# Performance work log

Measured on AMD Instinct MI355X. Metric: run time of the kernel, lower is better.

Reference implementation:

```python
import jax, jax.numpy as jnp
import numpy as np

EPS = 1e-5


def _bn(h, gamma, beta):
    # BatchNorm1d in training mode: batch statistics over node dim
    mu = h.mean(axis=0)
    var = h.var(axis=0)
    return gamma * (h - mu) * jax.lax.rsqrt(var + EPS) + beta


def _rgcn_layer(x, src, dst, etype, W, Wloop, b, n_dst):
    # Relation-specific gather-transform-scatter (DGL RelGraphConv, sum agg,
    # self-loop + bias, no regularizer).
    x_src = x[src]                                   # [E, in] gather
    num_rels = W.shape[0]
    m = jnp.zeros((x_src.shape[0], W.shape[2]), x.dtype)
    for r in range(num_rels):                        # small fixed relation count
        m = m + jnp.where((etype == r)[:, None], x_src @ W[r], 0.0)
    agg = jax.ops.segment_sum(m, dst, num_segments=n_dst)  # scatter-add to dst
    # DGL block convention: dst nodes are the prefix of src nodes
    return agg + x[:n_dst] @ Wloop + b


def setup_inputs() -> dict:
    key = jax.random.key(0)
    ks = jax.random.split(key, 16)
    N_SRC, N_DST0, N_DST1 = 200000, 50000, 10000
    E0, E1, R, H, C = 800000, 160000, 5, 256, 153
    s = 1.0 / np.sqrt(H)
    inp = {
        "x": jax.random.normal(ks[0], (N_SRC, H), jnp.float32),
        "src0": jax.random.randint(ks[1], (E0,), 0, N_SRC, jnp.int32),
        "dst0": jax.random.randint(ks[2], (E0,), 0, N_DST0, jnp.int32),
        "etype0": jax.random.randint(ks[3], (E0,), 0, R, jnp.int32),
        "src1": jax.random.randint(ks[4], (E1,), 0, N_DST0, jnp.int32),
        "dst1": jax.random.randint(ks[5], (E1,), 0, N_DST1, jnp.int32),
        "etype1": jax.random.randint(ks[6], (E1,), 0, R, jnp.int32),
        "n_dst0": N_DST0,
        "n_dst1": N_DST1,
        "W0": jax.random.normal(ks[7], (R, H, H), jnp.float32) * s,
        "Wl0": jax.random.normal(ks[8], (H, H), jnp.float32) * s,
        "b0": jnp.zeros((H,), jnp.float32),
        "g0": jnp.ones((H,), jnp.float32),
        "be0": jnp.zeros((H,), jnp.float32),
        "W1": jax.random.normal(ks[9], (R, H, H), jnp.float32) * s,
        "Wl1": jax.random.normal(ks[10], (H, H), jnp.float32) * s,
        "b1": jnp.zeros((H,), jnp.float32),
        "g1": jnp.ones((H,), jnp.float32),
        "be1": jnp.zeros((H,), jnp.float32),
        "Wm1": jax.random.normal(ks[11], (H, H), jnp.float32) * s,
        "bm1": jnp.zeros((H,), jnp.float32),
        "gm": jnp.ones((H,), jnp.float32),
        "bem": jnp.zeros((H,), jnp.float32),
        "Wm2": jax.random.normal(ks[12], (H, C), jnp.float32) * s,
        "bm2": jnp.zeros((C,), jnp.float32),
    }
    return inp


def reference(x, src0, dst0, etype0, src1, dst1, etype1, n_dst0, n_dst1,
              W0, Wl0, b0, g0, be0, W1, Wl1, b1, g1, be1,
              Wm1, bm1, gm, bem, Wm2, bm2):
    # layer 0
    h = _rgcn_layer(x, src0, dst0, etype0, W0, Wl0, b0, n_dst0)
    h = jax.nn.elu(_bn(h, g0, be0))
    # layer 1
    h = _rgcn_layer(h, src1, dst1, etype1, W1, Wl1, b1, n_dst1)
    h = jax.nn.elu(_bn(h, g1, be1))
    # MLP head (dropout is identity in eval)
    h = jax.nn.relu(_bn(h @ Wm1 + bm1, gm, bem))
    return h @ Wm2 + bm2
```

## Files before the change

### kernel.cpp

```cpp
#include <hip/hip_runtime.h>
#include <hip/hip_bf16.h>


#define HD   256
#define EPS  1e-5f
#define NREL 5
#define ND0  50000
#define ND1  10000
#define BK   64

typedef unsigned short ushort_t;
using f32x4  = __attribute__((ext_vector_type(4))) float;
using short8 = __attribute__((ext_vector_type(8))) short;

__device__ __forceinline__ ushort_t f2b(float f) {
    union { float f; unsigned u; } x; x.f = f;
    unsigned r = x.u + 0x7FFF + ((x.u >> 16) & 1);
    return (ushort_t)(r >> 16);
}
__device__ __forceinline__ float b2f(ushort_t h) {
    union { unsigned u; float f; } x; x.u = ((unsigned)h) << 16;
    return x.f;
}

#define GLOAD_LDS16(gp, lp)                                                     \
    __builtin_amdgcn_global_load_lds(                                           \
        (const __attribute__((address_space(1))) unsigned int*)(gp),            \
        (__attribute__((address_space(3))) unsigned int*)(lp), 16, 0, 0)

struct WconvArgs {
    const float* src[14];
    ushort_t*    dst[14];
    int          N[14];
};
__global__ void wconv_all_kernel(WconvArgs a) {
    int mat = blockIdx.x >> 8;
    int id = (blockIdx.x & 255) * 256 + threadIdx.x;
    int n = id >> 8, k = id & 255;
    int N = a.N[mat];
    float v = (n < N) ? a.src[mat][(size_t)k * N + n] : 0.f;
    a.dst[mat][id] = f2b(v);
}

__global__ void xconv_kernel(const float* __restrict__ x, ushort_t* __restrict__ xb,
                             int n4) {
    int id = blockIdx.x * 256 + threadIdx.x;
    if (id >= n4) return;
    float4 v = ((const float4*)x)[id];
    ushort4 o; o.x = f2b(v.x); o.y = f2b(v.y); o.z = f2b(v.z); o.w = f2b(v.w);
    ((ushort4*)xb)[id] = o;
}

__global__ void count2_kernel(const int* __restrict__ d0, const int* __restrict__ e0, int E0,
                              const int* __restrict__ d1, const int* __restrict__ e1, int E1,
                              int* __restrict__ cnt, int* __restrict__ pos) {
    int e = blockIdx.x * 256 + threadIdx.x;
    if (e < E0) {
        pos[e] = atomicAdd(&cnt[e0[e] * ND0 + d0[e]], 1);
    } else if (e < E0 + E1) {
        int i = e - E0;
        pos[e] = atomicAdd(&cnt[NREL * ND0 + e1[i] * ND1 + d1[i]], 1);
    }
}

__global__ void scan_block_kernel(const int* __restrict__ in, int* __restrict__ out,
                                  int* __restrict__ bsum, int nb) {
    __shared__ int ts[256];
    int tid = threadIdx.x;
    int base = blockIdx.x * 1024 + tid * 4;
    int v0 = (base + 0 < nb) ? in[base + 0] : 0;
    int v1 = (base + 1 < nb) ? in[base + 1] : 0;
    int v2 = (base + 2 < nb) ? in[base + 2] : 0;
    int v3 = (base + 3 < nb) ? in[base + 3] : 0;
    int tsum = v0 + v1 + v2 + v3;
    ts[tid] = tsum;
    __syncthreads();
    for (int d = 1; d < 256; d <<= 1) {
        int t = (tid >= d) ? ts[tid - d] : 0;
        __syncthreads();
        ts[tid] += t;
        __syncthreads();
    }
    int excl = ts[tid] - tsum;
    if (base + 0 < nb) out[base + 0] = excl;
    if (base + 1 < nb) out[base + 1] = excl + v0;
    if (base + 2 < nb) out[base + 2] = excl + v0 + v1;
    if (base + 3 < nb) out[base + 3] = excl + v0 + v1 + v2;
    if (tid == 255 && bsum) bsum[blockIdx.x] = ts[255];
}

__global__ void scan_add_kernel(int* __restrict__ out, const int* __restrict__ bsum, int nb) {
    int i = blockIdx.x * 256 + threadIdx.x;
    if (i < nb) out[i] += bsum[i >> 10];
}

__global__ void fill2_kernel(const int* __restrict__ s0, const int* __restrict__ d0,
                             const int* __restrict__ e0, int E0,
                             const int* __restrict__ s1, const int* __restrict__ d1,
                             const int* __restrict__ e1, int E1,
                             const int* __restrict__ pos, const int* __restrict__ off,
                             int* __restrict__ ssrc) {
    int e = blockIdx.x * 256 + threadIdx.x;
    if (e < E0) {
        ssrc[off[e0[e] * ND0 + d0[e]] + pos[e]] = s0[e];
    } else if (e < E0 + E1) {
        int i = e - E0;
        ssrc[off[NREL * ND0 + e1[i] * ND1 + d1[i]] + pos[e]] = s1[i];
    }
}

__global__ void gather_kernel(const ushort_t* __restrict__ feat, const int* __restrict__ ssrc,
                              const int* __restrict__ cnt, const int* __restrict__ off,
                              int nbuckets, ushort_t* __restrict__ out,
                              const float* __restrict__ sc, const float* __restrict__ sh) {
    int wave = (blockIdx.x * 256 + threadIdx.x) >> 6;
    int lane = threadIdx.x & 63;
    if (wave >= nbuckets) return;
    int deg = cnt[wave], s = off[wave];
    int half = lane >> 5;
    int cl = lane & 31;
    float a[8] = {0.f, 0.f, 0.f, 0.f, 0.f, 0.f, 0.f, 0.f};
    if (sc) {
        float4 s0v = ((const float4*)sc)[cl * 2], s1v = ((const float4*)sc)[cl * 2 + 1];
        float4 h0v = ((const float4*)sh)[cl * 2], h1v = ((const float4*)sh)[cl * 2 + 1];
        float scv[8] = {s0v.x, s0v.y, s0v.z, s0v.w, s1v.x, s1v.y, s1v.z, s1v.w};
        float shv[8] = {h0v.x, h0v.y, h0v.z, h0v.w, h1v.x, h1v.y, h1v.z, h1v.w};
        int j = half;
        for (; j + 2 < deg; j += 4) {
            int r0 = ssrc[s + j], r1 = ssrc[s + j + 2];
            uint4 v0 = *(const uint4*)(feat + (size_t)r0 * HD + cl * 8);
            uint4 v1 = *(const uint4*)(feat + (size_t)r1 * HD + cl * 8);
            const ushort_t* u0 = (const ushort_t*)&v0;
            const ushort_t* u1 = (const ushort_t*)&v1;
#pragma unroll
            for (int i = 0; i < 8; i++) {
                float f0 = fmaf(b2f(u0[i]), scv[i], shv[i]);
                float f1 = fmaf(b2f(u1[i]), scv[i], shv[i]);
                a[i] += (f0 > 0.f ? f0 : expm1f(f0)) + (f1 > 0.f ? f1 : expm1f(f1));
            }
        }
        if (j < deg) {
            int r = ssrc[s + j];
            uint4 v = *(const uint4*)(feat + (size_t)r * HD + cl * 8);
            const ushort_t* u = (const ushort_t*)&v;
#pragma unroll
            for (int i = 0; i < 8; i++) {
                float f = fmaf(b2f(u[i]), scv[i], shv[i]);
                a[i] += f > 0.f ? f : expm1f(f);
            }
        }
    } else {
        int j = half;
        for (; j + 2 < deg; j += 4) {
            int r0 = ssrc[s + j], r1 = ssrc[s + j + 2];
            uint4 v0 = *(const uint4*)(feat + (size_t)r0 * HD + cl * 8);
            uint4 v1 = *(const uint4*)(feat + (size_t)r1 * HD + cl * 8);
            const ushort_t* u0 = (const ushort_t*)&v0;
            const ushort_t* u1 = (const ushort_t*)&v1;
#pragma unroll
            for (int i = 0; i < 8; i++) a[i] += b2f(u0[i]) + b2f(u1[i]);
        }
        if (j < deg) {
            int r = ssrc[s + j];
            uint4 v = *(const uint4*)(feat + (size_t)r * HD + cl * 8);
            const ushort_t* u = (const ushort_t*)&v;
#pragma unroll
            for (int i = 0; i < 8; i++) a[i] += b2f(u[i]);
        }
    }
#pragma unroll
    for (int i = 0; i < 8; i++) a[i] += __shfl_xor(a[i], 32);
    if (half == 0) {
        ushort_t o[8];
#pragma unroll
        for (int i = 0; i < 8; i++) o[i] = f2b(a[i]);
        *(uint4*)(out + (size_t)wave * HD + cl * 8) = *(const uint4*)o;
    }
}

__global__ void bnprep_kernel(const float* __restrict__ sums, const float* __restrict__ g,
                              const float* __restrict__ be, float invM,
                              float* __restrict__ sc, float* __restrict__ sh) {
    int c = threadIdx.x;
    float mu = sums[c] * invM;
    float var = sums[HD + c] * invM - mu * mu;
    float s = g[c] * rsqrtf(var + EPS);
    sc[c] = s; sh[c] = be[c] - mu * s;
}

struct Seg {
    const ushort_t* A;
    const ushort_t* B;
    const float* sc;
    const float* sh;
    int act;
};
struct GemmArgs {
    Seg seg[6];
    int nseg;
    const float* bias;
    float* stats;
    ushort_t* Cb;
    float* Cf;
    int M, N;
};

template <int BM>
__launch_bounds__(256, 4)
__global__ void gemm_mfma_kernel(GemmArgs g) {
    constexpr int F   = BM / 32;
    constexpr int NFT = BM / 16;
    constexpr int IT  = NFT * 2 / 4;
    __shared__ __align__(1024) ushort_t As[NFT * 2 * 512];
    __shared__ __align__(1024) ushort_t Bs[NFT * 2 * 512];
    int tid = threadIdx.x;
    int wave = tid >> 6, lane = tid & 63;
    int rq = lane >> 4, ci = lane & 15;
    int wm = (wave >> 1) * (BM / 2), wn = (wave & 1) * (BM / 2);
    int bm = blockIdx.y * BM, bn = blockIdx.x * BM;
    f32x4 acc[F][F] = {};
    int K = g.nseg * HD;

    for (int kk = 0; kk < K; kk += BK) {
        int si = kk >> 8;
        int kl = kk & 255;
        const ushort_t* Ap = g.seg[si].A;
        const ushort_t* Bp = g.seg[si].B;
        const float* sc = g.seg[si].sc;
        if (!sc) {
#pragma unroll
            for (int it = 0; it < IT; it++) {
                int f = it * 4 + wave;
                int mt = f >> 1, kt = f & 1;
                const ushort_t* ga = Ap + (size_t)(bm + mt * 16 + ci) * HD
                                        + kl + kt * 32 + rq * 8;
                GLOAD_LDS16(ga, &As[f * 512 + lane * 8]);
            }
        } else {
            const float* sh = g.seg[si].sh;
            int act = g.seg[si].act;
#pragma unroll
            for (int it = 0; it < IT; it++) {
                int f = it * 4 + wave;
                int mt = f >> 1, kt = f & 1;
                int kb = kl + kt * 32 + rq * 8;
                uint4 v = *(const uint4*)(Ap + (size_t)(bm + mt * 16 + ci) * HD + kb);
                ushort_t* u = (ushort_t*)&v;
#pragma unroll
                for (int j = 0; j < 8; j++) {
                    float fv = fmaf(b2f(u[j]), sc[kb + j], sh[kb + j]);
                    fv = (act == 2) ? fmaxf(fv, 0.f) : (fv > 0.f ? fv : expm1f(fv));
                    u[j] = f2b(fv);
                }
                *(uint4*)&As[f * 512 + lane * 8] = v;
            }
        }
#pragma unroll
        for (int it = 0; it < IT; it++) {
            int f = it * 4 + wave;
            int nt = f >> 1, kt = f & 1;
            const ushort_t* gb = Bp + (size_t)(bn + nt * 16 + ci) * HD
                                    + kl + kt * 32 + rq * 8;
            GLOAD_LDS16(gb, &Bs[f * 512 + lane * 8]);
        }
        __syncthreads();
#pragma unroll
        for (int ks = 0; ks < 2; ks++) {
            short8 a[F], b[F];
#pragma unroll
            for (int mi = 0; mi < F; mi++)
                a[mi] = *(const short8*)&As[((wm / 16 + mi) * 2 + ks) * 512 + lane * 8];
#pragma unroll
            for (int ni = 0; ni < F; ni++)
                b[ni] = *(const short8*)&Bs[((wn / 16 + ni) * 2 + ks) * 512 + lane * 8];
#pragma unroll
            for (int mi = 0; mi < F; mi++)
#pragma unroll
                for (int ni = 0; ni < F; ni++)
                    acc[mi][ni] = __builtin_amdgcn_mfma_f32_16x16x32_bf16(
                        a[mi], b[ni], acc[mi][ni], 0, 0, 0);
        }
        __syncthreads();
    }

#pragma unroll
    for (int ni = 0; ni < F; ni++) {
        int col = bn + wn + ni * 16 + ci;
        float bv = (col < g.N) ? g.bias[col] : 0.f;
#pragma unroll
        for (int mi = 0; mi < F; mi++)
#pragma unroll
            for (int reg = 0; reg < 4; reg++) acc[mi][ni][reg] += bv;
    }
    if (g.stats) {
#pragma unroll
        for (int ni = 0; ni < F; ni++) {
            float s = 0.f, s2 = 0.f;
#pragma unroll
            for (int mi = 0; mi < F; mi++)
#pragma unroll
                for (int reg = 0; reg < 4; reg++) {
                    int row = bm + wm + mi * 16 + rq * 4 + reg;
                    if (row < g.M) { float v = acc[mi][ni][reg]; s += v; s2 += v * v; }
                }
            s  += __shfl_xor(s, 16);  s  += __shfl_xor(s, 32);
            s2 += __shfl_xor(s2, 16); s2 += __shfl_xor(s2, 32);
            if (rq == 0) {
                int col = bn + wn + ni * 16 + ci;
                atomicAdd(&g.stats[col], s);
                atomicAdd(&g.stats[HD + col], s2);
            }
        }
    }
#pragma unroll
    for (int mi = 0; mi < F; mi++)
#pragma unroll
        for (int ni = 0; ni < F; ni++)
#pragma unroll
            for (int reg = 0; reg < 4; reg++) {
                int row = bm + wm + mi * 16 + rq * 4 + reg;
                int col = bn + wn + ni * 16 + ci;
                if (row < g.M && col < g.N) {
                    float v = acc[mi][ni][reg];
                    if (g.Cb) g.Cb[(size_t)row * HD + col] = f2b(v);
                    else      g.Cf[(size_t)row * g.N + col] = v;
                }
            }
}

extern "C" void kernel_launch(void* const* d_in, const int* in_sizes, int n_in,
                              void* d_out, int out_size, void* d_ws, size_t ws_size,
                              hipStream_t stream) {
    const float* x   = (const float*)d_in[0];
    const int* src0  = (const int*)d_in[1];
    const int* dst0  = (const int*)d_in[2];
    const int* et0   = (const int*)d_in[3];
    const int* src1  = (const int*)d_in[4];
    const int* dst1  = (const int*)d_in[5];
    const int* et1   = (const int*)d_in[6];
    const float* W0  = (const float*)d_in[9];
    const float* Wl0 = (const float*)d_in[10];
    const float* b0  = (const float*)d_in[11];
    const float* g0  = (const float*)d_in[12];
    const float* be0 = (const float*)d_in[13];
    const float* W1  = (const float*)d_in[14];
    const float* Wl1 = (const float*)d_in[15];
    const float* b1  = (const float*)d_in[16];
    const float* g1  = (const float*)d_in[17];
    const float* be1 = (const float*)d_in[18];
    const float* Wm1 = (const float*)d_in[19];
    const float* bm1 = (const float*)d_in[20];
    const float* gm  = (const float*)d_in[21];
    const float* bem = (const float*)d_in[22];
    const float* Wm2 = (const float*)d_in[23];
    const float* bm2 = (const float*)d_in[24];

    const int E0 = in_sizes[1];
    const int E1 = in_sizes[4];
    const int NOUT = in_sizes[24];
    const int NSRC = in_sizes[0] / HD;
    const int NBKT = NREL * ND0 + NREL * ND1;

    char* p = (char*)d_ws;
    ushort_t* Wt = (ushort_t*)p;  p += (size_t)14 * 65536 * 2;
    float* st    = (float*)p;     p += 1536 * 4;
    float* bnp   = (float*)p;     p += 6 * 256 * 4;
    int* cnt     = (int*)p;       p += (size_t)NBKT * 4;
    int* off     = (int*)p;       p += (size_t)NBKT * 4;
    int* bsum    = (int*)p;       p += 1024 * 4;
    int* pos     = (int*)p;       p += (size_t)(E0 + E1) * 4;
    int* ssrc    = (int*)p;       p += (size_t)(E0 + E1) * 4;
    ushort_t* xb  = (ushort_t*)p; p += (size_t)NSRC * HD * 2;
    ushort_t* S0  = (ushort_t*)p; p += (size_t)(NREL * ND0 + 128) * HD * 2;
    ushort_t* S1  = (ushort_t*)p; p += (size_t)(NREL * ND1 + 128) * HD * 2;
    ushort_t* h0b = (ushort_t*)p; p += (size_t)(ND0 + 128) * HD * 2;
    ushort_t* h1b = (ushort_t*)p; p += (size_t)(ND1 + 128) * HD * 2;
    ushort_t* mb  = (ushort_t*)p; p += (size_t)(ND1 + 128) * HD * 2;

    float* st0 = st, *st1 = st + 512, *stm = st + 1024;
    float* sc0 = bnp, *sh0 = bnp + 256, *sc1 = bnp + 512, *sh1 = bnp + 768;
    float* scm = bnp + 1024, *shm = bnp + 1280;

    ushort_t* W0t  = Wt;
    ushort_t* Wl0t = Wt + 5 * 65536;
    ushort_t* W1t  = Wt + 6 * 65536;
    ushort_t* Wl1t = Wt + 11 * 65536;
    ushort_t* Wm1t = Wt + 12 * 65536;
    ushort_t* Wm2t = Wt + 13 * 65536;

    {
        WconvArgs wa;
        for (int r = 0; r < NREL; r++) { wa.src[r] = W0 + (size_t)r * 65536; wa.dst[r] = W0t + (size_t)r * 65536; wa.N[r] = 256; }
        wa.src[5] = Wl0; wa.dst[5] = Wl0t; wa.N[5] = 256;
        for (int r = 0; r < NREL; r++) { wa.src[6 + r] = W1 + (size_t)r * 65536; wa.dst[6 + r] = W1t + (size_t)r * 65536; wa.N[6 + r] = 256; }
        wa.src[11] = Wl1; wa.dst[11] = Wl1t; wa.N[11] = 256;
        wa.src[12] = Wm1; wa.dst[12] = Wm1t; wa.N[12] = 256;
        wa.src[13] = Wm2; wa.dst[13] = Wm2t; wa.N[13] = NOUT;
        wconv_all_kernel<<<14 * 256, 256, 0, stream>>>(wa);
    }
    xconv_kernel<<<(NSRC * 64 + 255) / 256, 256, 0, stream>>>(x, xb, NSRC * 64);
    hipMemsetAsync(st, 0, 1536 * sizeof(float), stream);
    hipMemsetAsync(cnt, 0, (size_t)NBKT * sizeof(int), stream);

    int ET = E0 + E1;
    count2_kernel<<<(ET + 255) / 256, 256, 0, stream>>>(dst0, et0, E0, dst1, et1, E1, cnt, pos);
    int nsb = (NBKT + 1023) / 1024;
    scan_block_kernel<<<nsb, 256, 0, stream>>>(cnt, off, bsum, NBKT);
    scan_block_kernel<<<1, 256, 0, stream>>>(bsum, bsum, nullptr, nsb);
    scan_add_kernel<<<(NBKT + 255) / 256, 256, 0, stream>>>(off, bsum, NBKT);
    fill2_kernel<<<(ET + 255) / 256, 256, 0, stream>>>(src0, dst0, et0, E0, src1, dst1, et1, E1, pos, off, ssrc);

    gather_kernel<<<(NREL * ND0 * 64) / 256, 256, 0, stream>>>(
        xb, ssrc, cnt, off, NREL * ND0, S0, nullptr, nullptr);
    {
        GemmArgs ga = {};
        for (int s = 0; s < NREL; s++)
            ga.seg[s] = { S0 + (size_t)s * ND0 * HD, W0t + (size_t)s * 65536, nullptr, nullptr, 0 };
        ga.seg[5] = { xb, Wl0t, nullptr, nullptr, 0 };
        ga.nseg = 6; ga.bias = b0; ga.stats = st0;
        ga.Cb = h0b; ga.Cf = nullptr; ga.M = ND0; ga.N = HD;
        gemm_mfma_kernel<128><<<dim3(2, (ND0 + 127) / 128), 256, 0, stream>>>(ga);
    }
    bnprep_kernel<<<1, 256, 0, stream>>>(st0, g0, be0, 1.f / ND0, sc0, sh0);

    gather_kernel<<<(NREL * ND1 * 64) / 256, 256, 0, stream>>>(
        h0b, ssrc, cnt + NREL * ND0, off + NREL * ND0, NREL * ND1, S1, sc0, sh0);
    {
        GemmArgs ga = {};
        for (int s = 0; s < NREL; s++)
            ga.seg[s] = { S1 + (size_t)s * ND1 * HD, W1t + (size_t)s * 65536, nullptr, nullptr, 0 };
        ga.seg[5] = { h0b, Wl1t, sc0, sh0, 1 };
        ga.nseg = 6; ga.bias = b1; ga.stats = st1;
        ga.Cb = h1b; ga.Cf = nullptr; ga.M = ND1; ga.N = HD;
        gemm_mfma_kernel<64><<<dim3(4, (ND1 + 63) / 64), 256, 0, stream>>>(ga);
    }
    bnprep_kernel<<<1, 256, 0, stream>>>(st1, g1, be1, 1.f / ND1, sc1, sh1);

    {
        GemmArgs ga = {};
        ga.seg[0] = { h1b, Wm1t, sc1, sh1, 1 };
        ga.nseg = 1; ga.bias = bm1; ga.stats = stm;
        ga.Cb = mb; ga.Cf = nullptr; ga.M = ND1; ga.N = HD;
        gemm_mfma_kernel<64><<<dim3(4, (ND1 + 63) / 64), 256, 0, stream>>>(ga);
    }
    bnprep_kernel<<<1, 256, 0, stream>>>(stm, gm, bem, 1.f / ND1, scm, shm);
    {
        GemmArgs ga = {};
        ga.seg[0] = { mb, Wm2t, scm, shm, 2 };
        ga.nseg = 1; ga.bias = bm2; ga.stats = nullptr;
        ga.Cb = nullptr; ga.Cf = (float*)d_out; ga.M = ND1; ga.N = NOUT;
        gemm_mfma_kernel<64><<<dim3((NOUT + 63) / 64, (ND1 + 63) / 64), 256, 0, stream>>>(ga);
    }
}
```

Measured before the change: 749.1 us.

## Fuse prep, memsets, scan-add and BN-prep into neighbouring kernels to cut launches

Merges weight conversion, x conversion and the two memsets into one prep kernel. The scan-add pass is dropped by adding the block sums on the fly in fill and gather. The three bnprep kernels are removed by recomputing BN scale and shift per block into shared memory inside the gather and GEMM kernels. This aims to cut launch count and small serial kernels, at the cost of redundant per-block BN-stat work and an extra bsum lookup per access.

```diff
diff --git a/kernel.cpp b/kernel.cpp
--- a/kernel.cpp
+++ b/kernel.cpp
@@ -33,22 +33,32 @@
     ushort_t*    dst[14];
     int          N[14];
 };
-__global__ void wconv_all_kernel(WconvArgs a) {
-    int mat = blockIdx.x >> 8;
-    int id = (blockIdx.x & 255) * 256 + threadIdx.x;
-    int n = id >> 8, k = id & 255;
-    int N = a.N[mat];
-    float v = (n < N) ? a.src[mat][(size_t)k * N + n] : 0.f;
-    a.dst[mat][id] = f2b(v);
-}
-
-__global__ void xconv_kernel(const float* __restrict__ x, ushort_t* __restrict__ xb,
-                             int n4) {
-    int id = blockIdx.x * 256 + threadIdx.x;
-    if (id >= n4) return;
-    float4 v = ((const float4*)x)[id];
-    ushort4 o; o.x = f2b(v.x); o.y = f2b(v.y); o.z = f2b(v.z); o.w = f2b(v.w);
-    ((ushort4*)xb)[id] = o;
+__global__ void prep_kernel(WconvArgs a, const float* __restrict__ x,
+                            ushort_t* __restrict__ xb, int n4,
+                            int* __restrict__ cnt, int ncnt4,
+                            float* __restrict__ st) {
+    int b = blockIdx.x;
+    int tid = threadIdx.x;
+    if (b < 3584) {
+        int mat = b >> 8;
+        int id = (b & 255) * 256 + tid;
+        int n = id >> 8, k = id & 255;
+        int N = a.N[mat];
+        float v = (n < N) ? a.src[mat][(size_t)k * N + n] : 0.f;
+        a.dst[mat][id] = f2b(v);
+    } else if (b < 53584) {
+        int id = (b - 3584) * 256 + tid;
+        if (id < n4) {
+            float4 v = ((const float4*)x)[id];
+            ushort4 o; o.x = f2b(v.x); o.y = f2b(v.y); o.z = f2b(v.z); o.w = f2b(v.w);
+            ((ushort4*)xb)[id] = o;
+        }
+    } else if (b < 53877) {
+        int id = (b - 53584) * 256 + tid;
+        if (id < ncnt4) ((int4*)cnt)[id] = make_int4(0, 0, 0, 0);
+    } else {
+        if (tid < 384) ((float4*)st)[tid] = make_float4(0.f, 0.f, 0.f, 0.f);
+    }
 }
 
 __global__ void count2_kernel(const int* __restrict__ d0, const int* __restrict__ e0, int E0,
@@ -89,40 +99,50 @@
     if (tid == 255 && bsum) bsum[blockIdx.x] = ts[255];
 }
 
-__global__ void scan_add_kernel(int* __restrict__ out, const int* __restrict__ bsum, int nb) {
-    int i = blockIdx.x * 256 + threadIdx.x;
-    if (i < nb) out[i] += bsum[i >> 10];
-}
-
 __global__ void fill2_kernel(const int* __restrict__ s0, const int* __restrict__ d0,
                              const int* __restrict__ e0, int E0,
                              const int* __restrict__ s1, const int* __restrict__ d1,
                              const int* __restrict__ e1, int E1,
                              const int* __restrict__ pos, const int* __restrict__ off,
+                             const int* __restrict__ bsum,
                              int* __restrict__ ssrc) {
     int e = blockIdx.x * 256 + threadIdx.x;
     if (e < E0) {
-        ssrc[off[e0[e] * ND0 + d0[e]] + pos[e]] = s0[e];
+        int bb = e0[e] * ND0 + d0[e];
+        ssrc[off[bb] + bsum[bb >> 10] + pos[e]] = s0[e];
     } else if (e < E0 + E1) {
         int i = e - E0;
-        ssrc[off[NREL * ND0 + e1[i] * ND1 + d1[i]] + pos[e]] = s1[i];
+        int bb = NREL * ND0 + e1[i] * ND1 + d1[i];
+        ssrc[off[bb] + bsum[bb >> 10] + pos[e]] = s1[i];
     }
 }
 
 __global__ void gather_kernel(const ushort_t* __restrict__ feat, const int* __restrict__ ssrc,
                               const int* __restrict__ cnt, const int* __restrict__ off,
+                              const int* __restrict__ bsum, int bktbase,
                               int nbuckets, ushort_t* __restrict__ out,
-                              const float* __restrict__ sc, const float* __restrict__ sh) {
+                              const float* __restrict__ bnst, const float* __restrict__ bng,
+                              const float* __restrict__ bnbe, float bninv) {
+    __shared__ float scL[256], shL[256];
+    if (bnst) {
+        int c = threadIdx.x;
+        float mu = bnst[c] * bninv;
+        float var = bnst[HD + c] * bninv - mu * mu;
+        float s = bng[c] * rsqrtf(var + EPS);
+        scL[c] = s; shL[c] = bnbe[c] - mu * s;
+        __syncthreads();
+    }
     int wave = (blockIdx.x * 256 + threadIdx.x) >> 6;
     int lane = threadIdx.x & 63;
     if (wave >= nbuckets) return;
-    int deg = cnt[wave], s = off[wave];
+    int gb = bktbase + wave;
+    int deg = cnt[gb], s = off[gb] + bsum[gb >> 10];
     int half = lane >> 5;
     int cl = lane & 31;
     float a[8] = {0.f, 0.f, 0.f, 0.f, 0.f, 0.f, 0.f, 0.f};
-    if (sc) {
-        float4 s0v = ((const float4*)sc)[cl * 2], s1v = ((const float4*)sc)[cl * 2 + 1];
-        float4 h0v = ((const float4*)sh)[cl * 2], h1v = ((const float4*)sh)[cl * 2 + 1];
+    if (bnst) {
+        float4 s0v = ((const float4*)scL)[cl * 2], s1v = ((const float4*)scL)[cl * 2 + 1];
+        float4 h0v = ((const float4*)shL)[cl * 2], h1v = ((const float4*)shL)[cl * 2 + 1];
         float scv[8] = {s0v.x, s0v.y, s0v.z, s0v.w, s1v.x, s1v.y, s1v.z, s1v.w};
         float shv[8] = {h0v.x, h0v.y, h0v.z, h0v.w, h1v.x, h1v.y, h1v.z, h1v.w};
         int j = half;
@@ -178,26 +198,19 @@
     }
 }
 
-__global__ void bnprep_kernel(const float* __restrict__ sums, const float* __restrict__ g,
-                              const float* __restrict__ be, float invM,
-                              float* __restrict__ sc, float* __restrict__ sh) {
-    int c = threadIdx.x;
-    float mu = sums[c] * invM;
-    float var = sums[HD + c] * invM - mu * mu;
-    float s = g[c] * rsqrtf(var + EPS);
-    sc[c] = s; sh[c] = be[c] - mu * s;
-}
-
 struct Seg {
     const ushort_t* A;
     const ushort_t* B;
-    const float* sc;
-    const float* sh;
-    int act;
 };
 struct GemmArgs {
     Seg seg[6];
     int nseg;
+    int fseg;
+    int fact;
+    const float* fst;
+    const float* fg;
+    const float* fbe;
+    float finv;
     const float* bias;
     float* stats;
     ushort_t* Cb;
@@ -213,7 +226,16 @@
     constexpr int IT  = NFT * 2 / 4;
     __shared__ __align__(1024) ushort_t As[NFT * 2 * 512];
     __shared__ __align__(1024) ushort_t Bs[NFT * 2 * 512];
+    __shared__ float scL[256], shL[256];
     int tid = threadIdx.x;
+    if (g.fseg >= 0) {
+        int c = tid;
+        float mu = g.fst[c] * g.finv;
+        float var = g.fst[HD + c] * g.finv - mu * mu;
+        float s = g.fg[c] * rsqrtf(var + EPS);
+        scL[c] = s; shL[c] = g.fbe[c] - mu * s;
+        __syncthreads();
+    }
     int wave = tid >> 6, lane = tid & 63;
     int rq = lane >> 4, ci = lane & 15;
     int wm = (wave >> 1) * (BM / 2), wn = (wave & 1) * (BM / 2);
@@ -226,8 +248,7 @@
         int kl = kk & 255;
         const ushort_t* Ap = g.seg[si].A;
         const ushort_t* Bp = g.seg[si].B;
-        const float* sc = g.seg[si].sc;
-        if (!sc) {
+        if (si != g.fseg) {
 #pragma unroll
             for (int it = 0; it < IT; it++) {
                 int f = it * 4 + wave;
@@ -237,8 +258,7 @@
                 GLOAD_LDS16(ga, &As[f * 512 + lane * 8]);
             }
         } else {
-            const float* sh = g.seg[si].sh;
-            int act = g.seg[si].act;
+            int act = g.fact;
 #pragma unroll
             for (int it = 0; it < IT; it++) {
                 int f = it * 4 + wave;
@@ -248,7 +268,7 @@
                 ushort_t* u = (ushort_t*)&v;
 #pragma unroll
                 for (int j = 0; j < 8; j++) {
-                    float fv = fmaf(b2f(u[j]), sc[kb + j], sh[kb + j]);
+                    float fv = fmaf(b2f(u[j]), scL[kb + j], shL[kb + j]);
                     fv = (act == 2) ? fmaxf(fv, 0.f) : (fv > 0.f ? fv : expm1f(fv));
                     u[j] = f2b(fv);
                 }
@@ -364,7 +384,6 @@
     char* p = (char*)d_ws;
     ushort_t* Wt = (ushort_t*)p;  p += (size_t)14 * 65536 * 2;
     float* st    = (float*)p;     p += 1536 * 4;
-    float* bnp   = (float*)p;     p += 6 * 256 * 4;
     int* cnt     = (int*)p;       p += (size_t)NBKT * 4;
     int* off     = (int*)p;       p += (size_t)NBKT * 4;
     int* bsum    = (int*)p;       p += 1024 * 4;
@@ -378,8 +397,6 @@
     ushort_t* mb  = (ushort_t*)p; p += (size_t)(ND1 + 128) * HD * 2;
 
     float* st0 = st, *st1 = st + 512, *stm = st + 1024;
-    float* sc0 = bnp, *sh0 = bnp + 256, *sc1 = bnp + 512, *sh1 = bnp + 768;
-    float* scm = bnp + 1024, *shm = bnp + 1280;
 
     ushort_t* W0t  = Wt;
     ushort_t* Wl0t = Wt + 5 * 65536;
@@ -396,58 +413,59 @@
         wa.src[11] = Wl1; wa.dst[11] = Wl1t; wa.N[11] = 256;
         wa.src[12] = Wm1; wa.dst[12] = Wm1t; wa.N[12] = 256;
         wa.src[13] = Wm2; wa.dst[13] = Wm2t; wa.N[13] = NOUT;
-        wconv_all_kernel<<<14 * 256, 256, 0, stream>>>(wa);
-    }
-    xconv_kernel<<<(NSRC * 64 + 255) / 256, 256, 0, stream>>>(x, xb, NSRC * 64);
-    hipMemsetAsync(st, 0, 1536 * sizeof(float), stream);
-    hipMemsetAsync(cnt, 0, (size_t)NBKT * sizeof(int), stream);
+        int n4 = NSRC * 64;
+        prep_kernel<<<53878, 256, 0, stream>>>(wa, x, xb, n4, cnt, NBKT / 4, st);
+    }
 
     int ET = E0 + E1;
     count2_kernel<<<(ET + 255) / 256, 256, 0, stream>>>(dst0, et0, E0, dst1, et1, E1, cnt, pos);
     int nsb = (NBKT + 1023) / 1024;
     scan_block_kernel<<<nsb, 256, 0, stream>>>(cnt, off, bsum, NBKT);
     scan_block_kernel<<<1, 256, 0, stream>>>(bsum, bsum, nullptr, nsb);
-    scan_add_kernel<<<(NBKT + 255) / 256, 256, 0, stream>>>(off, bsum, NBKT);
-    fill2_kernel<<<(ET + 255) / 256, 256, 0, stream>>>(src0, dst0, et0, E0, src1, dst1, et1, E1, pos, off, ssrc);
+    fill2_kernel<<<(ET + 255) / 256, 256, 0, stream>>>(src0, dst0, et0, E0, src1, dst1, et1, E1, pos, off, bsum, ssrc);
 
     gather_kernel<<<(NREL * ND0 * 64) / 256, 256, 0, stream>>>(
-        xb, ssrc, cnt, off, NREL * ND0, S0, nullptr, nullptr);
+        xb, ssrc, cnt, off, bsum, 0, NREL * ND0, S0, nullptr, nullptr, nullptr, 0.f);
     {
         GemmArgs ga = {};
         for (int s = 0; s < NREL; s++)
-            ga.seg[s] = { S0 + (size_t)s * ND0 * HD, W0t + (size_t)s * 65536, nullptr, nullptr, 0 };
-        ga.seg[5] = { xb, Wl0t, nullptr, nullptr, 0 };
-        ga.nseg = 6; ga.bias = b0; ga.stats = st0;
+            ga.seg[s] = { S0 + (size_t)s * ND0 * HD, W0t + (size_t)s * 65536 };
+        ga.seg[5] = { xb, Wl0t };
+        ga.nseg = 6; ga.fseg = -1;
+        ga.bias = b0; ga.stats = st0;
         ga.Cb = h0b; ga.Cf = nullptr; ga.M = ND0; ga.N = HD;
         gemm_mfma_kernel<128><<<dim3(2, (ND0 + 127) / 128), 256, 0, stream>>>(ga);
     }
-    bnprep_kernel<<<1, 256, 0, stream>>>(st0, g0, be0, 1.f / ND0, sc0, sh0);
 
     gather_kernel<<<(NREL * ND1 * 64) / 256, 256, 0, stream>>>(
-        h0b, ssrc, cnt + NREL * ND0, off + NREL * ND0, NREL * ND1, S1, sc0, sh0);
+        h0b, ssrc, cnt, off, bsum, NREL * ND0, NREL * ND1, S1, st0, g0, be0, 1.f / ND0);
     {
         GemmArgs ga = {};
         for (int s = 0; s < NREL; s++)
-            ga.seg[s] = { S1 + (size_t)s * ND1 * HD, W1t + (size_t)s * 65536, nullptr, nullptr, 0 };
-        ga.seg[5] = { h0b, Wl1t, sc0, sh0, 1 };
-        ga.nseg = 6; ga.bias = b1; ga.stats = st1;
+            ga.seg[s] = { S1 + (size_t)s * ND1 * HD, W1t + (size_t)s * 65536 };
+        ga.seg[5] = { h0b, Wl1t };
+        ga.nseg = 6; ga.fseg = 5; ga.fact = 1;
+        ga.fst = st0; ga.fg = g0; ga.fbe = be0; ga.finv = 1.f / ND0;
+        ga.bias = b1; ga.stats = st1;
         ga.Cb = h1b; ga.Cf = nullptr; ga.M = ND1; ga.N = HD;
         gemm_mfma_kernel<64><<<dim3(4, (ND1 + 63) / 64), 256, 0, stream>>>(ga);
     }
-    bnprep_kernel<<<1, 256, 0, stream>>>(st1, g1, be1, 1.f / ND1, sc1, sh1);
 
     {
         GemmArgs ga = {};
-        ga.seg[0] = { h1b, Wm1t, sc1, sh1, 1 };
-        ga.nseg = 1; ga.bias = bm1; ga.stats = stm;
+        ga.seg[0] = { h1b, Wm1t };
+        ga.nseg = 1; ga.fseg = 0; ga.fact = 1;
+        ga.fst = st1; ga.fg = g1; ga.fbe = be1; ga.finv = 1.f / ND1;
+        ga.bias = bm1; ga.stats = stm;
         ga.Cb = mb; ga.Cf = nullptr; ga.M = ND1; ga.N = HD;
         gemm_mfma_kernel<64><<<dim3(4, (ND1 + 63) / 64), 256, 0, stream>>>(ga);
     }
-    bnprep_kernel<<<1, 256, 0, stream>>>(stm, gm, bem, 1.f / ND1, scm, shm);
     {
         GemmArgs ga = {};
-        ga.seg[0] = { mb, Wm2t, scm, shm, 2 };
-        ga.nseg = 1; ga.bias = bm2; ga.stats = nullptr;
+        ga.seg[0] = { mb, Wm2t };
+        ga.nseg = 1; ga.fseg = 0; ga.fact = 2;
+        ga.fst = stm; ga.fg = gm; ga.fbe = bem; ga.finv = 1.f / ND1;
+        ga.bias = bm2; ga.stats = nullptr;
         ga.Cb = nullptr; ga.Cf = (float*)d_out; ga.M = ND1; ga.N = NOUT;
         gemm_mfma_kernel<64><<<dim3((NOUT + 63) / 64, (ND1 + 63) / 64), 256, 0, stream>>>(ga);
     }
```

New measurement: 737.4 us. Within noise of the previous version (-1.6%).
